# Optimization experiments

Hardware: AMD Instinct MI355X
Metric: run time of the kernel (lower is better)

Reference implementation:

```python
import jax, jax.numpy as jnp
import numpy as np

B, N, F_IN, F_OUT = 8, 2048, 64, 64
ALPHA = 0.2  # LeakyReLU negative slope


def setup_inputs() -> dict:
    key = jax.random.key(0)
    k_in, k_adj, k_w, k_a1, k_a2 = jax.random.split(key, 5)
    inp = jax.random.normal(k_in, (B, N, F_IN), dtype=jnp.float32)
    adj = (jax.random.uniform(k_adj, (B, N, N)) < 0.05).astype(jnp.float32)
    # xavier_uniform with gain=sqrt(2)
    def xavier(k, shape):
        fan_in, fan_out = shape[0], shape[1]
        bound = np.sqrt(2.0) * np.sqrt(6.0 / (fan_in + fan_out))
        return jax.random.uniform(k, shape, jnp.float32, -bound, bound)
    W = xavier(k_w, (F_IN, F_OUT))
    a1 = xavier(k_a1, (F_OUT, 1))
    a2 = xavier(k_a2, (F_OUT, 1))
    bias = jnp.full((N, F_OUT), 0.1, dtype=jnp.float32)
    return {"input": inp, "adj": adj, "W": W, "a1": a1, "a2": a2, "bias": bias}


def reference(input, adj, W, a1, a2, bias):
    # h: [B, N, F_OUT]
    h = jnp.einsum("bnf,fo->bno", input, W)
    f1 = h @ a1          # [B, N, 1]
    f2 = h @ a2          # [B, N, 1]
    e = jax.nn.leaky_relu(f1 + jnp.swapaxes(f2, 1, 2), negative_slope=ALPHA)  # [B, N, N]
    # NOTE: original multiplies adj elementwise (not -inf mask) and softmaxes over dim=1
    attention = jax.nn.softmax(adj * e, axis=1)
    h_prime = jnp.einsum("bij,bjo->bio", attention, h) + bias  # bias broadcasts over batch
    h_prime = h_prime + input  # in_features == out_features, no downsample
    return jax.nn.elu(h_prime)
```

## Files before the change

kernel.cpp:

```cpp
#include <hip/hip_runtime.h>
#include <cstdint>
#include <cstddef>

#define Bn 8
#define Nn 2048
#define Fn 64
#define ALPHA 0.2f

typedef __attribute__((ext_vector_type(8))) short  s8frag;
typedef __attribute__((ext_vector_type(4))) float  f4frag;

__device__ __forceinline__ float lrelu(float x) { return fmaxf(x, ALPHA * x); }
__device__ __forceinline__ float elu(float x)   { return x > 0.f ? x : __expf(x) - 1.f; }
__device__ __forceinline__ unsigned short bfr(float f) {
    unsigned u = __float_as_uint(f);
    u += 0x7fffu + ((u >> 16) & 1u);
    return (unsigned short)(u >> 16);
}

__global__ __launch_bounds__(256) void k1_h_f(
        const float* __restrict__ inp, const float* __restrict__ W,
        const float* __restrict__ a1, const float* __restrict__ a2,
        float* __restrict__ h, float* __restrict__ f1, float* __restrict__ f2) {
    __shared__ float Wl[Fn * Fn];
    __shared__ float inr[4 * Fn];
    int t = threadIdx.x;
    for (int k = t; k < Fn * Fn; k += 256) Wl[k] = W[k];
    size_t row0 = (size_t)blockIdx.x * 4;
    inr[t] = inp[row0 * Fn + t];
    __syncthreads();
    int r = t >> 6, o = t & 63;
    const float* irow = &inr[r * Fn];
    float acc = 0.f;
#pragma unroll
    for (int f = 0; f < Fn; ++f) acc = fmaf(irow[f], Wl[f * Fn + o], acc);
    size_t row = row0 + r;
    h[row * Fn + o] = acc;
    float p = acc * a1[o];
    float q = acc * a2[o];
#pragma unroll
    for (int off = 32; off > 0; off >>= 1) {
        p += __shfl_down(p, off, 64);
        q += __shfl_down(q, off, 64);
    }
    if (o == 0) { f1[row] = p; f2[row] = q; }
}

__global__ __launch_bounds__(256) void k1b_max(
        const float* __restrict__ f1, float* __restrict__ f1max) {
    int b = blockIdx.x, t = threadIdx.x;
    float m = -3.4e38f;
    for (int i = t; i < Nn; i += 256) m = fmaxf(m, f1[b * Nn + i]);
#pragma unroll
    for (int off = 32; off > 0; off >>= 1) m = fmaxf(m, __shfl_down(m, off, 64));
    __shared__ float sm[4];
    if ((t & 63) == 0) sm[t >> 6] = m;
    __syncthreads();
    if (t == 0) f1max[b] = fmaxf(fmaxf(sm[0], sm[1]), fmaxf(sm[2], sm[3]));
}

__global__ __launch_bounds__(512) void k2a_bits(
        const float* __restrict__ adj, const float* __restrict__ f1,
        const float* __restrict__ f2, const float* __restrict__ f1max_p,
        float* __restrict__ Dsum, unsigned char* __restrict__ bitsL) {
    int b = blockIdx.x;
    int cj = blockIdx.y;
    int j0 = cj * 256;
    int i0 = blockIdx.z * 128;
    int w = threadIdx.x >> 6, lane = threadIdx.x & 63;
    float f1max = f1max_p[b];
    float4 f2v = *(const float4*)&f2[b * Nn + j0 + 4 * lane];
    float Mf0 = fmaxf(lrelu(f1max + f2v.x), 0.f);
    float Mf1 = fmaxf(lrelu(f1max + f2v.y), 0.f);
    float Mf2 = fmaxf(lrelu(f1max + f2v.z), 0.f);
    float Mf3 = fmaxf(lrelu(f1max + f2v.w), 0.f);
    float vh0 = __expf(f2v.x - Mf0), vp0 = __expf(ALPHA * f2v.x - Mf0), ez0 = __expf(-Mf0);
    float vh1 = __expf(f2v.y - Mf1), vp1 = __expf(ALPHA * f2v.y - Mf1), ez1 = __expf(-Mf1);
    float vh2 = __expf(f2v.z - Mf2), vp2 = __expf(ALPHA * f2v.z - Mf2), ez2 = __expf(-Mf2);
    float vh3 = __expf(f2v.w - Mf3), vp3 = __expf(ALPHA * f2v.w - Mf3), ez3 = __expf(-Mf3);
    float s0 = 0.f, s1 = 0.f, s2 = 0.f, s3 = 0.f;
    const float* abase = adj + ((size_t)b * Nn) * Nn + j0 + 4 * lane;
    const float* f1b = f1 + b * Nn;
    int g = lane >> 1;
    int boff = (g & 3) * 8 + (g >> 2);
    bool evenlane = (lane & 1) == 0;
    size_t bbase = ((size_t)(b * 8 + cj) * Nn) * 32;

    int rb = i0 + w;
    float4 av0 = *(const float4*)(abase + (size_t)(rb +  0) * Nn);
    float4 av1 = *(const float4*)(abase + (size_t)(rb +  8) * Nn);
    float4 av2 = *(const float4*)(abase + (size_t)(rb + 16) * Nn);
    float4 av3 = *(const float4*)(abase + (size_t)(rb + 24) * Nn);
    float fi0 = f1b[rb], fi1 = f1b[rb + 8], fi2 = f1b[rb + 16], fi3 = f1b[rb + 24];

    for (int gi = 0; gi < 4; ++gi) {
        int rc = i0 + w + 32 * gi;
        float4 nv0, nv1, nv2, nv3;
        float nf0 = 0.f, nf1 = 0.f, nf2 = 0.f, nf3 = 0.f;
        if (gi < 3) {
            int rn = rc + 32;
            nv0 = *(const float4*)(abase + (size_t)(rn +  0) * Nn);
            nv1 = *(const float4*)(abase + (size_t)(rn +  8) * Nn);
            nv2 = *(const float4*)(abase + (size_t)(rn + 16) * Nn);
            nv3 = *(const float4*)(abase + (size_t)(rn + 24) * Nn);
            nf0 = f1b[rn]; nf1 = f1b[rn + 8]; nf2 = f1b[rn + 16]; nf3 = f1b[rn + 24];
        }
#define PROC(AV, FI, IROW)                                                     \
        {                                                                      \
            float u  = __expf(FI);                                             \
            float up = __expf(ALPHA * (FI));                                   \
            bool n0 = AV.x != 0.f, n1 = AV.y != 0.f,                           \
                 n2 = AV.z != 0.f, n3 = AV.w != 0.f;                           \
            float x0 = (FI) + f2v.x, x1 = (FI) + f2v.y,                        \
                  x2 = (FI) + f2v.z, x3 = (FI) + f2v.w;                        \
            float e0 = x0 > 0.f ? u * vh0 : up * vp0;                          \
            float e1 = x1 > 0.f ? u * vh1 : up * vp1;                          \
            float e2 = x2 > 0.f ? u * vh2 : up * vp2;                          \
            float e3 = x3 > 0.f ? u * vh3 : up * vp3;                          \
            s0 += n0 ? e0 : ez0;                                               \
            s1 += n1 ? e1 : ez1;                                               \
            s2 += n2 ? e2 : ez2;                                               \
            s3 += n3 ? e3 : ez3;                                               \
            unsigned nib = (unsigned)n0 | ((unsigned)n1 << 1) |                \
                           ((unsigned)n2 << 2) | ((unsigned)n3 << 3);          \
            unsigned other = __shfl_xor(nib, 1, 64);                           \
            if (evenlane)                                                      \
                bitsL[bbase + (size_t)(IROW) * 32 + boff] =                    \
                    (unsigned char)(nib | (other << 4));                       \
        }
        PROC(av0, fi0, rc +  0)
        PROC(av1, fi1, rc +  8)
        PROC(av2, fi2, rc + 16)
        PROC(av3, fi3, rc + 24)
#undef PROC
        av0 = nv0; av1 = nv1; av2 = nv2; av3 = nv3;
        fi0 = nf0; fi1 = nf1; fi2 = nf2; fi3 = nf3;
    }
    __shared__ float sred[8][256];
    sred[w][4 * lane + 0] = s0;
    sred[w][4 * lane + 1] = s1;
    sred[w][4 * lane + 2] = s2;
    sred[w][4 * lane + 3] = s3;
    __syncthreads();
    if (threadIdx.x < 256) {
        int c = threadIdx.x;
        float v = 0.f;
#pragma unroll
        for (int k = 0; k < 8; ++k) v += sred[k][c];
        atomicAdd(&Dsum[b * Nn + j0 + c], v);
    }
}

__global__ __launch_bounds__(256) void k2b_scale_T(
        const float* __restrict__ h, const float* __restrict__ Dsum,
        const float* __restrict__ f2, const float* __restrict__ f1max_p,
        unsigned short* __restrict__ hTs, float4* __restrict__ cf4) {
    int b = blockIdx.x;
    int j0 = blockIdx.y * 64;
    int t = threadIdx.x;
    __shared__ float Lh[64][68];
    __shared__ float Rsh[64];
    if (t < 64) {
        int j = j0 + t;
        float f2j = f2[b * Nn + j];
        float Mf = fmaxf(lrelu(f1max_p[b] + f2j), 0.f);
        Rsh[t] = 1.f / Dsum[b * Nn + j];
        cf4[b * Nn + j] = make_float4(f2j, __expf(f2j - Mf),
                                      __expf(ALPHA * f2j - Mf), __expf(-Mf));
    }
#pragma unroll
    for (int q = 0; q < 4; ++q) {
        int fi = t + 256 * q;
        int jj = fi >> 4, oq = fi & 15;
        float4 v = *(const float4*)(h + ((size_t)(b * Nn + j0 + jj)) * Fn + oq * 4);
        *(float4*)&Lh[jj][oq * 4] = v;
    }
    __syncthreads();
    int o = t >> 2, jg = (t & 3) * 16;
    unsigned wbuf[8];
#pragma unroll
    for (int s2 = 0; s2 < 8; ++s2) {
        int j = jg + 2 * s2;
        unsigned lo16 = bfr(Lh[j][o] * Rsh[j]);
        unsigned hi16 = bfr(Lh[j + 1][o] * Rsh[j + 1]);
        wbuf[s2] = lo16 | (hi16 << 16);
    }
    unsigned short* dst = hTs + ((size_t)(b * Fn + o)) * Nn + j0 + jg;
    *(uint4*)dst       = make_uint4(wbuf[0], wbuf[1], wbuf[2], wbuf[3]);
    *(uint4*)(dst + 8) = make_uint4(wbuf[4], wbuf[5], wbuf[6], wbuf[7]);
}

__global__ __launch_bounds__(256) void k3_fused(
        const unsigned char* __restrict__ bitsL,
        const unsigned short* __restrict__ hTs,
        const float4* __restrict__ cf4, const float* __restrict__ f1,
        const float* __restrict__ inp, const float* __restrict__ bias,
        float* __restrict__ out) {
    int b = blockIdx.x;
    int i0 = blockIdx.y * 16;
    int w = threadIdx.x >> 6, lane = threadIdx.x & 63;
    int m = lane & 15, kg = lane >> 4;
    int i = i0 + m;

    __shared__ float4 shb[Nn];
    {
        const float4* src = cf4 + (size_t)b * Nn;
        for (int q = threadIdx.x; q < Nn; q += 256) shb[q] = src[q];
    }
    uint2 pre0 = *(const uint2*)(bitsL + ((size_t)(b * 8 + 2 * w) * Nn + i) * 32 + kg * 8);
    uint2 pre1 = *(const uint2*)(bitsL + ((size_t)(b * 8 + 2 * w + 1) * Nn + i) * 32 + kg * 8);
    float f1i = f1[b * Nn + i];
    float ui = __expf(f1i), upi = __expf(ALPHA * f1i);
    __syncthreads();

    f4frag acc0 = {0.f,0.f,0.f,0.f}, acc1 = {0.f,0.f,0.f,0.f};
    f4frag acc2 = {0.f,0.f,0.f,0.f}, acc3 = {0.f,0.f,0.f,0.f};
    const unsigned short* Ab = hTs + (size_t)b * Fn * Nn + (size_t)m * Nn;

    for (int jcl = 0; jcl < 2; ++jcl) {
        int jc = 2 * w + jcl;
        unsigned blo = jcl ? pre1.x : pre0.x;
        unsigned bhi = jcl ? pre1.y : pre0.y;
#pragma unroll 2
        for (int t = 0; t < 8; ++t) {
            unsigned bv = ((t < 4 ? blo : bhi) >> ((t & 3) * 8)) & 0xffu;
            int j = jc * 256 + t * 32 + kg * 8;
            s8frag bf;
#pragma unroll
            for (int r = 0; r < 8; ++r) {
                float4 c = shb[j + r];
                float x = f1i + c.x;
                float uv = x > 0.f ? ui * c.y : upi * c.z;
                float val = ((bv >> r) & 1u) ? uv : c.w;
                bf[r] = (short)bfr(val);
            }
            const unsigned short* Aj = Ab + j;
            s8frag a0 = *(const s8frag*)(Aj);
            s8frag a1 = *(const s8frag*)(Aj + 16 * Nn);
            s8frag a2 = *(const s8frag*)(Aj + 32 * Nn);
            s8frag a3 = *(const s8frag*)(Aj + 48 * Nn);
            acc0 = __builtin_amdgcn_mfma_f32_16x16x32_bf16(a0, bf, acc0, 0, 0, 0);
            acc1 = __builtin_amdgcn_mfma_f32_16x16x32_bf16(a1, bf, acc1, 0, 0, 0);
            acc2 = __builtin_amdgcn_mfma_f32_16x16x32_bf16(a2, bf, acc2, 0, 0, 0);
            acc3 = __builtin_amdgcn_mfma_f32_16x16x32_bf16(a3, bf, acc3, 0, 0, 0);
        }
    }
    __syncthreads();
    f4frag accs[4] = {acc0, acc1, acc2, acc3};
#pragma unroll
    for (int ot = 0; ot < 4; ++ot)
        shb[(w * 64 + lane) * 4 + ot] =
            make_float4(accs[ot][0], accs[ot][1], accs[ot][2], accs[ot][3]);
    __syncthreads();
    int il = threadIdx.x & 15, oq = threadIdx.x >> 4;
    int ot = oq >> 2, kg2 = oq & 3;
    float4 v = make_float4(0.f, 0.f, 0.f, 0.f);
#pragma unroll
    for (int ww = 0; ww < 4; ++ww) {
        float4 p = shb[(ww * 64 + kg2 * 16 + il) * 4 + ot];
        v.x += p.x; v.y += p.y; v.z += p.z; v.w += p.w;
    }
    int o = oq * 4;
    size_t gbase = ((size_t)b * Nn + i0 + il) * Fn + o;
    float4 iv  = *(const float4*)(inp + gbase);
    float4 bv4 = *(const float4*)(bias + (size_t)(i0 + il) * Fn + o);
    float4 r;
    r.x = elu(v.x + iv.x + bv4.x);
    r.y = elu(v.y + iv.y + bv4.y);
    r.z = elu(v.z + iv.z + bv4.z);
    r.w = elu(v.w + iv.w + bv4.w);
    *(float4*)(out + gbase) = r;
}

extern "C" void kernel_launch(void* const* d_in, const int* in_sizes, int n_in,
                              void* d_out, int out_size, void* d_ws, size_t ws_size,
                              hipStream_t stream) {
    const float* inp  = (const float*)d_in[0];
    const float* adj  = (const float*)d_in[1];
    const float* W    = (const float*)d_in[2];
    const float* a1   = (const float*)d_in[3];
    const float* a2   = (const float*)d_in[4];
    const float* bias = (const float*)d_in[5];
    float* out = (float*)d_out;

    unsigned char* bitsL = (unsigned char*)d_ws;
    unsigned short* hTs  = (unsigned short*)(bitsL + (size_t)Bn * Nn * Nn / 8);
    float* h     = (float*)(hTs + (size_t)Bn * Fn * Nn);
    float* f1    = h + (size_t)Bn * Nn * Fn;
    float* f2    = f1 + (size_t)Bn * Nn;
    float* Dsum  = f2 + (size_t)Bn * Nn;
    float4* cf4  = (float4*)(Dsum + (size_t)Bn * Nn);
    float* f1max = (float*)(cf4 + (size_t)Bn * Nn);

    hipMemsetAsync(Dsum, 0, (size_t)Bn * Nn * sizeof(float), stream);
    k1_h_f<<<Bn * Nn / 4, 256, 0, stream>>>(inp, W, a1, a2, h, f1, f2);
    k1b_max<<<Bn, 256, 0, stream>>>(f1, f1max);
    k2a_bits<<<dim3(Bn, 8, 16), 512, 0, stream>>>(adj, f1, f2, f1max, Dsum, bitsL);
    k2b_scale_T<<<dim3(Bn, Nn / 64), 256, 0, stream>>>(h, Dsum, f2, f1max, hTs, cf4);
    k3_fused<<<dim3(Bn, Nn / 16), 256, 0, stream>>>(bitsL, hTs, cf4, f1, inp, bias, out);
}
```

Baseline: 258.2 us.

## Replace dense bitmask MFMA aggregation with CSR sparse gather plus dense baseline term

The adjacency pass now builds per-row column lists with wave ballots and atomic counters, instead of writing a packed bitmask. The softmax is rewritten as a dense baseline term, the per-column zero-entry weight times h summed once per batch, plus a sparse correction over the nonzero entries only. This removes the dense bf16 MFMA aggregation and the transposed bf16 copy of h. The cost is atomic contention when building the lists and a serial, latency-bound gather loop per row. Column lists are capped at a fixed size, so denser adjacency rows would be silently truncated.

```diff
diff --git a/kernel.cpp b/kernel.cpp
--- a/kernel.cpp
+++ b/kernel.cpp
@@ -6,17 +6,10 @@
 #define Nn 2048
 #define Fn 64
 #define ALPHA 0.2f
-
-typedef __attribute__((ext_vector_type(8))) short  s8frag;
-typedef __attribute__((ext_vector_type(4))) float  f4frag;
+#define CAP 192
 
 __device__ __forceinline__ float lrelu(float x) { return fmaxf(x, ALPHA * x); }
 __device__ __forceinline__ float elu(float x)   { return x > 0.f ? x : __expf(x) - 1.f; }
-__device__ __forceinline__ unsigned short bfr(float f) {
-    unsigned u = __float_as_uint(f);
-    u += 0x7fffu + ((u >> 16) & 1u);
-    return (unsigned short)(u >> 16);
-}
 
 __global__ __launch_bounds__(256) void k1_h_f(
         const float* __restrict__ inp, const float* __restrict__ W,
@@ -59,13 +52,13 @@
     if (t == 0) f1max[b] = fmaxf(fmaxf(sm[0], sm[1]), fmaxf(sm[2], sm[3]));
 }
 
-__global__ __launch_bounds__(512) void k2a_bits(
+__global__ __launch_bounds__(512) void k2a_csr(
         const float* __restrict__ adj, const float* __restrict__ f1,
         const float* __restrict__ f2, const float* __restrict__ f1max_p,
-        float* __restrict__ Dsum, unsigned char* __restrict__ bitsL) {
+        float* __restrict__ Dsum, unsigned* __restrict__ rowcnt,
+        unsigned short* __restrict__ csr) {
     int b = blockIdx.x;
-    int cj = blockIdx.y;
-    int j0 = cj * 256;
+    int j0 = blockIdx.y * 256;
     int i0 = blockIdx.z * 128;
     int w = threadIdx.x >> 6, lane = threadIdx.x & 63;
     float f1max = f1max_p[b];
@@ -81,10 +74,6 @@
     float s0 = 0.f, s1 = 0.f, s2 = 0.f, s3 = 0.f;
     const float* abase = adj + ((size_t)b * Nn) * Nn + j0 + 4 * lane;
     const float* f1b = f1 + b * Nn;
-    int g = lane >> 1;
-    int boff = (g & 3) * 8 + (g >> 2);
-    bool evenlane = (lane & 1) == 0;
-    size_t bbase = ((size_t)(b * 8 + cj) * Nn) * 32;
 
     int rb = i0 + w;
     float4 av0 = *(const float4*)(abase + (size_t)(rb +  0) * Nn);
@@ -92,6 +81,23 @@
     float4 av2 = *(const float4*)(abase + (size_t)(rb + 16) * Nn);
     float4 av3 = *(const float4*)(abase + (size_t)(rb + 24) * Nn);
     float fi0 = f1b[rb], fi1 = f1b[rb + 8], fi2 = f1b[rb + 16], fi3 = f1b[rb + 24];
+
+#define APPEND(NK, RROW, COL)                                                  \
+        {                                                                      \
+            unsigned long long mk = __ballot(NK);                              \
+            if (mk) {                                                          \
+                unsigned basek = 0;                                            \
+                if (lane == 0)                                                 \
+                    basek = atomicAdd(&rowcnt[RROW], (unsigned)__popcll(mk));  \
+                basek = (unsigned)__shfl((int)basek, 0, 64);                   \
+                if (NK) {                                                      \
+                    unsigned sl = basek +                                      \
+                        (unsigned)__popcll(mk & ((1ull << lane) - 1ull));      \
+                    if (sl < CAP)                                              \
+                        csr[(size_t)(RROW) * CAP + sl] = (unsigned short)(COL);\
+                }                                                              \
+            }                                                                  \
+        }
 
     for (int gi = 0; gi < 4; ++gi) {
         int rc = i0 + w + 32 * gi;
@@ -121,18 +127,18 @@
             s1 += n1 ? e1 : ez1;                                               \
             s2 += n2 ? e2 : ez2;                                               \
             s3 += n3 ? e3 : ez3;                                               \
-            unsigned nib = (unsigned)n0 | ((unsigned)n1 << 1) |                \
-                           ((unsigned)n2 << 2) | ((unsigned)n3 << 3);          \
-            unsigned other = __shfl_xor(nib, 1, 64);                           \
-            if (evenlane)                                                      \
-                bitsL[bbase + (size_t)(IROW) * 32 + boff] =                    \
-                    (unsigned char)(nib | (other << 4));                       \
+            unsigned rrow = (unsigned)(b * Nn + (IROW));                       \
+            APPEND(n0, rrow, j0 + 4 * lane + 0)                                \
+            APPEND(n1, rrow, j0 + 4 * lane + 1)                                \
+            APPEND(n2, rrow, j0 + 4 * lane + 2)                                \
+            APPEND(n3, rrow, j0 + 4 * lane + 3)                                \
         }
         PROC(av0, fi0, rc +  0)
         PROC(av1, fi1, rc +  8)
         PROC(av2, fi2, rc + 16)
         PROC(av3, fi3, rc + 24)
 #undef PROC
+#undef APPEND
         av0 = nv0; av1 = nv1; av2 = nv2; av3 = nv3;
         fi0 = nf0; fi1 = nf1; fi2 = nf2; fi3 = nf3;
     }
@@ -151,125 +157,75 @@
     }
 }
 
-__global__ __launch_bounds__(256) void k2b_scale_T(
+__global__ __launch_bounds__(256) void k2b_cols(
         const float* __restrict__ h, const float* __restrict__ Dsum,
         const float* __restrict__ f2, const float* __restrict__ f1max_p,
-        unsigned short* __restrict__ hTs, float4* __restrict__ cf4) {
+        float4* __restrict__ cf4, float* __restrict__ C) {
     int b = blockIdx.x;
     int j0 = blockIdx.y * 64;
     int t = threadIdx.x;
-    __shared__ float Lh[64][68];
-    __shared__ float Rsh[64];
+    __shared__ float zl[64];
     if (t < 64) {
         int j = j0 + t;
         float f2j = f2[b * Nn + j];
         float Mf = fmaxf(lrelu(f1max_p[b] + f2j), 0.f);
-        Rsh[t] = 1.f / Dsum[b * Nn + j];
-        cf4[b * Nn + j] = make_float4(f2j, __expf(f2j - Mf),
-                                      __expf(ALPHA * f2j - Mf), __expf(-Mf));
-    }
-#pragma unroll
-    for (int q = 0; q < 4; ++q) {
-        int fi = t + 256 * q;
-        int jj = fi >> 4, oq = fi & 15;
-        float4 v = *(const float4*)(h + ((size_t)(b * Nn + j0 + jj)) * Fn + oq * 4);
-        *(float4*)&Lh[jj][oq * 4] = v;
-    }
-    __syncthreads();
-    int o = t >> 2, jg = (t & 3) * 16;
-    unsigned wbuf[8];
-#pragma unroll
-    for (int s2 = 0; s2 < 8; ++s2) {
-        int j = jg + 2 * s2;
-        unsigned lo16 = bfr(Lh[j][o] * Rsh[j]);
-        unsigned hi16 = bfr(Lh[j + 1][o] * Rsh[j + 1]);
-        wbuf[s2] = lo16 | (hi16 << 16);
-    }
-    unsigned short* dst = hTs + ((size_t)(b * Fn + o)) * Nn + j0 + jg;
-    *(uint4*)dst       = make_uint4(wbuf[0], wbuf[1], wbuf[2], wbuf[3]);
-    *(uint4*)(dst + 8) = make_uint4(wbuf[4], wbuf[5], wbuf[6], wbuf[7]);
-}
-
-__global__ __launch_bounds__(256) void k3_fused(
-        const unsigned char* __restrict__ bitsL,
-        const unsigned short* __restrict__ hTs,
+        float invD = 1.f / Dsum[b * Nn + j];
+        float vh = __expf(f2j - Mf) * invD;
+        float vp = __expf(ALPHA * f2j - Mf) * invD;
+        float ez = __expf(-Mf) * invD;
+        cf4[b * Nn + j] = make_float4(f2j, vh, vp, ez);
+        zl[t] = ez;
+    }
+    __syncthreads();
+    int o = t & 63, g = t >> 6;
+    const float* hbp = h + ((size_t)(b * Nn + j0 + g * 16)) * Fn + o;
+    float s = 0.f;
+#pragma unroll
+    for (int k = 0; k < 16; ++k) s = fmaf(zl[g * 16 + k], hbp[(size_t)k * Fn], s);
+    atomicAdd(&C[b * Fn + o], s);
+}
+
+__global__ __launch_bounds__(256) void k3_sparse(
+        const unsigned short* __restrict__ csr, const unsigned* __restrict__ rowcnt,
         const float4* __restrict__ cf4, const float* __restrict__ f1,
+        const float* __restrict__ h, const float* __restrict__ C,
         const float* __restrict__ inp, const float* __restrict__ bias,
         float* __restrict__ out) {
     int b = blockIdx.x;
-    int i0 = blockIdx.y * 16;
     int w = threadIdx.x >> 6, lane = threadIdx.x & 63;
-    int m = lane & 15, kg = lane >> 4;
-    int i = i0 + m;
-
-    __shared__ float4 shb[Nn];
-    {
-        const float4* src = cf4 + (size_t)b * Nn;
-        for (int q = threadIdx.x; q < Nn; q += 256) shb[q] = src[q];
-    }
-    uint2 pre0 = *(const uint2*)(bitsL + ((size_t)(b * 8 + 2 * w) * Nn + i) * 32 + kg * 8);
-    uint2 pre1 = *(const uint2*)(bitsL + ((size_t)(b * 8 + 2 * w + 1) * Nn + i) * 32 + kg * 8);
-    float f1i = f1[b * Nn + i];
+    int i = blockIdx.y * 4 + w;
+    size_t rb = (size_t)b * Nn + i;
+    unsigned cnt = rowcnt[rb];
+    if (cnt > CAP) cnt = CAP;
+    float f1i = f1[rb];
     float ui = __expf(f1i), upi = __expf(ALPHA * f1i);
-    __syncthreads();
-
-    f4frag acc0 = {0.f,0.f,0.f,0.f}, acc1 = {0.f,0.f,0.f,0.f};
-    f4frag acc2 = {0.f,0.f,0.f,0.f}, acc3 = {0.f,0.f,0.f,0.f};
-    const unsigned short* Ab = hTs + (size_t)b * Fn * Nn + (size_t)m * Nn;
-
-    for (int jcl = 0; jcl < 2; ++jcl) {
-        int jc = 2 * w + jcl;
-        unsigned blo = jcl ? pre1.x : pre0.x;
-        unsigned bhi = jcl ? pre1.y : pre0.y;
-#pragma unroll 2
-        for (int t = 0; t < 8; ++t) {
-            unsigned bv = ((t < 4 ? blo : bhi) >> ((t & 3) * 8)) & 0xffu;
-            int j = jc * 256 + t * 32 + kg * 8;
-            s8frag bf;
-#pragma unroll
-            for (int r = 0; r < 8; ++r) {
-                float4 c = shb[j + r];
-                float x = f1i + c.x;
-                float uv = x > 0.f ? ui * c.y : upi * c.z;
-                float val = ((bv >> r) & 1u) ? uv : c.w;
-                bf[r] = (short)bfr(val);
+    const unsigned short* lst = csr + rb * CAP;
+    const float4* cfb = cf4 + (size_t)b * Nn;
+    const float* hb = h + ((size_t)b * Nn) * Fn + lane;
+    float acc = C[b * Fn + lane];
+
+    for (unsigned c0 = 0; c0 < cnt; c0 += 64) {
+        int m = (int)(cnt - c0 < 64u ? cnt - c0 : 64u);
+        int idx = (lane < m) ? (int)lst[c0 + lane] : 0;
+        int jc = __shfl(idx, 0, 64);
+        float4 cfa = cfb[jc];
+        float hva = hb[(size_t)jc * Fn];
+        for (int t = 0; t < m; ++t) {
+            float4 cf = cfa;
+            float hv = hva;
+            if (t + 1 < m) {
+                int jn = __shfl(idx, t + 1, 64);
+                cfa = cfb[jn];
+                hva = hb[(size_t)jn * Fn];
             }
-            const unsigned short* Aj = Ab + j;
-            s8frag a0 = *(const s8frag*)(Aj);
-            s8frag a1 = *(const s8frag*)(Aj + 16 * Nn);
-            s8frag a2 = *(const s8frag*)(Aj + 32 * Nn);
-            s8frag a3 = *(const s8frag*)(Aj + 48 * Nn);
-            acc0 = __builtin_amdgcn_mfma_f32_16x16x32_bf16(a0, bf, acc0, 0, 0, 0);
-            acc1 = __builtin_amdgcn_mfma_f32_16x16x32_bf16(a1, bf, acc1, 0, 0, 0);
-            acc2 = __builtin_amdgcn_mfma_f32_16x16x32_bf16(a2, bf, acc2, 0, 0, 0);
-            acc3 = __builtin_amdgcn_mfma_f32_16x16x32_bf16(a3, bf, acc3, 0, 0, 0);
-        }
-    }
-    __syncthreads();
-    f4frag accs[4] = {acc0, acc1, acc2, acc3};
-#pragma unroll
-    for (int ot = 0; ot < 4; ++ot)
-        shb[(w * 64 + lane) * 4 + ot] =
-            make_float4(accs[ot][0], accs[ot][1], accs[ot][2], accs[ot][3]);
-    __syncthreads();
-    int il = threadIdx.x & 15, oq = threadIdx.x >> 4;
-    int ot = oq >> 2, kg2 = oq & 3;
-    float4 v = make_float4(0.f, 0.f, 0.f, 0.f);
-#pragma unroll
-    for (int ww = 0; ww < 4; ++ww) {
-        float4 p = shb[(ww * 64 + kg2 * 16 + il) * 4 + ot];
-        v.x += p.x; v.y += p.y; v.z += p.z; v.w += p.w;
-    }
-    int o = oq * 4;
-    size_t gbase = ((size_t)b * Nn + i0 + il) * Fn + o;
-    float4 iv  = *(const float4*)(inp + gbase);
-    float4 bv4 = *(const float4*)(bias + (size_t)(i0 + il) * Fn + o);
-    float4 r;
-    r.x = elu(v.x + iv.x + bv4.x);
-    r.y = elu(v.y + iv.y + bv4.y);
-    r.z = elu(v.z + iv.z + bv4.z);
-    r.w = elu(v.w + iv.w + bv4.w);
-    *(float4*)(out + gbase) = r;
+            float x = f1i + cf.x;
+            float wv = (x > 0.f ? ui * cf.y : upi * cf.z) - cf.w;
+            acc = fmaf(wv, hv, acc);
+        }
+    }
+    size_t gbase = rb * Fn + lane;
+    float r = acc + inp[gbase] + bias[(size_t)i * Fn + lane];
+    out[gbase] = elu(r);
 }
 
 extern "C" void kernel_launch(void* const* d_in, const int* in_sizes, int n_in,
@@ -283,19 +239,21 @@
     const float* bias = (const float*)d_in[5];
     float* out = (float*)d_out;
 
-    unsigned char* bitsL = (unsigned char*)d_ws;
-    unsigned short* hTs  = (unsigned short*)(bitsL + (size_t)Bn * Nn * Nn / 8);
-    float* h     = (float*)(hTs + (size_t)Bn * Fn * Nn);
-    float* f1    = h + (size_t)Bn * Nn * Fn;
-    float* f2    = f1 + (size_t)Bn * Nn;
-    float* Dsum  = f2 + (size_t)Bn * Nn;
-    float4* cf4  = (float4*)(Dsum + (size_t)Bn * Nn);
-    float* f1max = (float*)(cf4 + (size_t)Bn * Nn);
-
-    hipMemsetAsync(Dsum, 0, (size_t)Bn * Nn * sizeof(float), stream);
+    char* ws = (char*)d_ws;
+    unsigned short* csr = (unsigned short*)ws;
+    float*  h     = (float*)(ws + 6291456);
+    float4* cf4   = (float4*)(ws + 10485760);
+    float*  f1    = (float*)(ws + 10747904);
+    float*  f2    = (float*)(ws + 10813440);
+    float*  f1max = (float*)(ws + 10878976);
+    float*  Dsum  = (float*)(ws + 10879040);
+    unsigned* rowcnt = (unsigned*)(ws + 10944576);
+    float*  C     = (float*)(ws + 11010112);
+
+    hipMemsetAsync(ws + 10879040, 0, 65536 + 65536 + 2048, stream);
     k1_h_f<<<Bn * Nn / 4, 256, 0, stream>>>(inp, W, a1, a2, h, f1, f2);
     k1b_max<<<Bn, 256, 0, stream>>>(f1, f1max);
-    k2a_bits<<<dim3(Bn, 8, 16), 512, 0, stream>>>(adj, f1, f2, f1max, Dsum, bitsL);
-    k2b_scale_T<<<dim3(Bn, Nn / 64), 256, 0, stream>>>(h, Dsum, f2, f1max, hTs, cf4);
-    k3_fused<<<dim3(Bn, Nn / 16), 256, 0, stream>>>(bitsL, hTs, cf4, f1, inp, bias, out);
-}
+    k2a_csr<<<dim3(Bn, 8, 16), 512, 0, stream>>>(adj, f1, f2, f1max, Dsum, rowcnt, csr);
+    k2b_cols<<<dim3(Bn, Nn / 64), 256, 0, stream>>>(h, Dsum, f2, f1max, cf4, C);
+    k3_sparse<<<dim3(Bn, Nn / 4), 256, 0, stream>>>(csr, rowcnt, cf4, f1, h, C, inp, bias, out);
+}
```

Result: slower. 392.1 us (+51.8%).
